# Kernel optimization log

Hardware: AMD Instinct MI355X
Metric: run time of the kernel (lower is better)

## Reference

```python
import jax, jax.numpy as jnp
import numpy as np
import math

D_MODEL = 1024
N_HEAD = 16
Q_DIM = K_DIM = V_DIM = 1024
SCALE = math.sqrt(D_MODEL // N_HEAD)  # 8.0
B, LQ, LK = 2, 2048, 2048


def setup_inputs() -> dict:
    key = jax.random.key(0)
    ks = jax.random.split(key, 10)
    s = 1.0 / math.sqrt(Q_DIM)
    return {
        "q": jax.random.normal(ks[0], (B, LQ, Q_DIM), jnp.float32),
        "k": jax.random.normal(ks[1], (B, LK, K_DIM), jnp.float32),
        "v": jax.random.normal(ks[2], (B, LK, V_DIM), jnp.float32),
        "mask": jax.random.randint(ks[3], (B, LQ, LK), 0, 2, jnp.int32),
        "Wq": jax.random.uniform(ks[4], (D_MODEL, Q_DIM), jnp.float32, -s, s),
        "bq": jnp.zeros((D_MODEL,), jnp.float32),
        "Wk": jax.random.uniform(ks[5], (D_MODEL, K_DIM), jnp.float32, -s, s),
        "bk": jnp.zeros((D_MODEL,), jnp.float32),
        "Wv": jax.random.uniform(ks[6], (D_MODEL, V_DIM), jnp.float32, -s, s),
        "bv": jnp.zeros((D_MODEL,), jnp.float32),
    }


def reference(q, k, v, Wq, bq, Wk, bk, Wv, bv, mask):
    b, lq, _ = q.shape
    lk = k.shape[1]
    dh = D_MODEL // N_HEAD
    # linear projections (torch Linear: x @ W.T + b)
    qh = (q @ Wq.T + bq).reshape(b, lq, N_HEAD, dh).transpose(0, 2, 1, 3)  # bhqd
    kh = (k @ Wk.T + bk).reshape(b, lk, N_HEAD, dh).transpose(0, 2, 1, 3)  # bhkd
    vh = (v @ Wv.T + bv).reshape(b, lk, N_HEAD, dh).transpose(0, 2, 1, 3)  # bhkd
    attn = jnp.einsum("bhqd,bhkd->bhqk", qh, kh) / SCALE
    m = mask[:, None, :, :]  # b1qk
    attn = jnp.where(m == 0, -jnp.inf, attn)
    # rows whose mask is all-zero are reset to 0 pre-softmax (-> uniform weights)
    row_empty = (m.sum(-1, keepdims=True) == 0)
    attn = jnp.where(row_empty, 0.0, attn)
    attn = jax.nn.softmax(attn, axis=-1)  # dropout is identity in eval mode
    v_out = jnp.einsum("bhqk,bhkd->bhqd", attn, vh)
    v_out = v_out.transpose(0, 2, 1, 3).reshape(b, lq, D_MODEL)
    k_out = jnp.einsum("bhqk,bhkd->bhqd", attn, kh)
    k_out = k_out.transpose(0, 2, 1, 3).reshape(b, lq, D_MODEL)
    return (k_out, v_out)
```

## Files before the change

### kernel.cpp

```cpp
#include <hip/hip_runtime.h>
#include <hip/hip_bf16.h>
#include <stdint.h>

typedef __bf16 bf16x8 __attribute__((ext_vector_type(8)));
typedef __bf16 bf16x4 __attribute__((ext_vector_type(4)));
typedef float f32x4 __attribute__((ext_vector_type(4)));

#define B_ 2
#define LQ_ 2048
#define LK_ 2048
#define NH_ 16
#define DH_ 64
#define DM_ 1024
#define NKT_ (LK_ / 64)

#define AS1 __attribute__((address_space(1)))
#define AS3 __attribute__((address_space(3)))

__device__ __forceinline__ void gload_lds16(const void* g, void* l) {
  __builtin_amdgcn_global_load_lds((const AS1 uint32_t*)g, (AS3 uint32_t*)l, 16, 0, 0);
}

__global__ __launch_bounds__(256) void prep_kernel(
    const float* __restrict__ q, const float* __restrict__ k,
    const float* __restrict__ v, const float* __restrict__ wq,
    const float* __restrict__ wk, const float* __restrict__ wv,
    const int* __restrict__ mask,
    __bf16* __restrict__ Xt0, __bf16* __restrict__ Xt1, __bf16* __restrict__ Xt2,
    __bf16* __restrict__ Wt0, __bf16* __restrict__ Wt1, __bf16* __restrict__ Wt2,
    unsigned* __restrict__ maskp) {
  const int t = threadIdx.x;
  const int bidx = blockIdx.x;
  if (bidx >= 960) {
    int pb = bidx - 960;
    int lane = t & 63;
    size_t gi = ((size_t)pb * 256 + t) * 4;
    int4 mv = *(const int4*)(mask + gi);
    unsigned nib = (mv.x != 0 ? 1u : 0u) | (mv.y != 0 ? 2u : 0u) |
                   (mv.z != 0 ? 4u : 0u) | (mv.w != 0 ? 8u : 0u);
    unsigned vv = nib << ((lane & 7) * 4);
    vv |= __shfl_xor(vv, 1, 64);
    vv |= __shfl_xor(vv, 2, 64);
    vv |= __shfl_xor(vv, 4, 64);
    if ((lane & 7) == 0) maskp[gi >> 5] = vv;
    return;
  }
  __shared__ __align__(16) __bf16 lb[16][1032];
  const float* src; __bf16* dst; int rows, m0;
  if (bidx < 256)      { src = q;  dst = Xt0; rows = 4096; m0 = bidx * 16; }
  else if (bidx < 512) { src = k;  dst = Xt1; rows = 4096; m0 = (bidx - 256) * 16; }
  else if (bidx < 768) { src = v;  dst = Xt2; rows = 4096; m0 = (bidx - 512) * 16; }
  else if (bidx < 832) { src = wq; dst = Wt0; rows = 1024; m0 = (bidx - 768) * 16; }
  else if (bidx < 896) { src = wk; dst = Wt1; rows = 1024; m0 = (bidx - 832) * 16; }
  else                 { src = wv; dst = Wt2; rows = 1024; m0 = (bidx - 896) * 16; }
#pragma unroll
  for (int i = 0; i < 16; i++) {
    float4 f = *(const float4*)(src + (size_t)(m0 + i) * DM_ + t * 4);
    bf16x4 o;
    o[0] = (__bf16)f.x; o[1] = (__bf16)f.y; o[2] = (__bf16)f.z; o[3] = (__bf16)f.w;
    *(bf16x4*)&lb[i][t * 4] = o;
  }
  __syncthreads();
  const int wave = t >> 6, lane = t & 63;
  const int m = lane >> 2, c = lane & 3;
#pragma unroll
  for (int j = 0; j < 8; j++) {
    int kt = wave * 8 + j;
    bf16x8 val = *(const bf16x8*)&lb[m][kt * 32 + (c ^ (m & 3)) * 8];
    *(bf16x8*)(dst + ((size_t)kt * rows + m0 + m) * 32 + c * 8) = val;
  }
}

__global__ __launch_bounds__(256) void proj_kernel(
    const __bf16* __restrict__ Xt0, const __bf16* __restrict__ Xt1,
    const __bf16* __restrict__ Xt2,
    const float* __restrict__ b0p, const float* __restrict__ b1p,
    const float* __restrict__ b2p,
    const __bf16* __restrict__ Wt0, const __bf16* __restrict__ Wt1,
    const __bf16* __restrict__ Wt2,
    __bf16* __restrict__ qh, __bf16* __restrict__ kh,
    __bf16* __restrict__ khT, __bf16* __restrict__ vhT) {
  __shared__ __align__(16) __bf16 smem[2][2][128 * 32];
  __bf16* cbuf = &smem[0][0][0];

  const int mode = blockIdx.z;
  const __bf16* Xt = mode == 0 ? Xt0 : (mode == 1 ? Xt1 : Xt2);
  const __bf16* Wt = mode == 0 ? Wt0 : (mode == 1 ? Wt1 : Wt2);
  const float* bias = mode == 0 ? b0p : (mode == 1 ? b1p : b2p);
  __bf16* ostd = mode == 0 ? qh : (mode == 1 ? kh : nullptr);
  __bf16* otr = mode == 0 ? nullptr : (mode == 1 ? khT : vhT);
  const float osc = mode == 0 ? 0.18033688f : 1.0f;

  const int t = threadIdx.x;
  const int wave = t >> 6, lane = t & 63;
  const int lo16 = lane & 15, quad = lane >> 4;
  const int wm = wave >> 1, wn = wave & 1;
  const int m0 = blockIdx.x * 128, n0 = blockIdx.y * 128;

  f32x4 acc[4][4] = {};

  auto stage = [&](int kt, int sel) {
#pragma unroll
    for (int ii = 2 * wave; ii < 2 * wave + 2; ii++) {
      gload_lds16(Xt + ((size_t)kt * 4096 + m0 + ii * 16) * 32 + lane * 8,
                  &smem[sel][0][ii * 512]);
      gload_lds16(Wt + ((size_t)kt * 1024 + n0 + ii * 16) * 32 + lane * 8,
                  &smem[sel][1][ii * 512]);
    }
  };

  stage(0, 0);
  for (int kt = 0; kt < 32; kt++) {
    const int sel = kt & 1;
    __syncthreads();
    if (kt + 1 < 32) stage(kt + 1, sel ^ 1);
    bf16x8 af[4], bfr[4];
#pragma unroll
    for (int g = 0; g < 4; g++) {
      int ar = wm * 64 + g * 16 + lo16;
      af[g] = *(const bf16x8*)(&smem[sel][0][ar * 32 + (quad ^ (ar & 3)) * 8]);
      int br = wn * 64 + g * 16 + lo16;
      bfr[g] = *(const bf16x8*)(&smem[sel][1][br * 32 + (quad ^ (br & 3)) * 8]);
    }
#pragma unroll
    for (int gm = 0; gm < 4; gm++)
#pragma unroll
      for (int gn = 0; gn < 4; gn++)
        acc[gm][gn] =
            __builtin_amdgcn_mfma_f32_16x16x32_bf16(af[gm], bfr[gn], acc[gm][gn], 0, 0, 0);
  }

  const int b = m0 >> 11, l0 = m0 & 2047;
  for (int nhf = 0; nhf < 2; nhf++) {
    int h = (n0 >> 6) + nhf;
    int bh = b * NH_ + h;
    if (ostd) {
      __syncthreads();
      if (wn == nhf) {
#pragma unroll
        for (int gn = 0; gn < 4; gn++) {
          float bi = bias[n0 + nhf * 64 + gn * 16 + lo16];
#pragma unroll
          for (int gm = 0; gm < 4; gm++)
#pragma unroll
            for (int r = 0; r < 4; r++)
              cbuf[(wm * 64 + gm * 16 + quad * 4 + r) * 72 + gn * 16 + lo16] =
                  (__bf16)((acc[gm][gn][r] + bi) * osc);
        }
      }
      __syncthreads();
      int m = t >> 1, coff = (t & 1) * 32;
      __bf16* dst = ostd + ((size_t)bh * LQ_ + l0 + m) * DH_ + coff;
#pragma unroll
      for (int j = 0; j < 4; j++)
        *(bf16x8*)(dst + j * 8) = *(const bf16x8*)&cbuf[m * 72 + coff + j * 8];
    }
    if (otr) {
      __syncthreads();
      if (wn == nhf) {
#pragma unroll
        for (int gn = 0; gn < 4; gn++) {
          float bi = bias[n0 + nhf * 64 + gn * 16 + lo16];
#pragma unroll
          for (int gm = 0; gm < 4; gm++) {
            bf16x4 pk;
#pragma unroll
            for (int r = 0; r < 4; r++) pk[r] = (__bf16)(acc[gm][gn][r] + bi);
            *(bf16x4*)&cbuf[(gn * 16 + lo16) * 136 + wm * 64 + gm * 16 + quad * 4] = pk;
          }
        }
      }
      __syncthreads();
      int d = t >> 2, mc = (t & 3) * 32;
      int kti = (l0 + mc) >> 6, kl = (l0 + mc) & 63;
      __bf16* dst = otr + ((size_t)(bh * NKT_ + kti) * 64 + d) * 64 + kl;
#pragma unroll
      for (int j = 0; j < 4; j++)
        *(bf16x8*)(dst + j * 8) = *(const bf16x8*)&cbuf[d * 136 + mc + j * 8];
    }
  }
}

__global__ __launch_bounds__(512) void attn_kernel(
    const __bf16* __restrict__ qh, const __bf16* __restrict__ kh,
    const __bf16* __restrict__ khT, const __bf16* __restrict__ vhT,
    const unsigned* __restrict__ maskp,
    float* __restrict__ out_k, float* __restrict__ out_v) {
  __shared__ __align__(16) __bf16 kbuf[2][64 * 64];
  __shared__ __align__(16) __bf16 ktbuf[2][64 * 64];
  __shared__ __align__(16) __bf16 vtbuf[2][64 * 64];
  __shared__ __align__(16) __bf16 p_lds[8][16][72];

  const int t = threadIdx.x;
  const int wave = t >> 6, lane = t & 63;
  const int lo16 = lane & 15, quad = lane >> 4;
  const int bh = blockIdx.x;
  const int b = bh >> 4, h = bh & 15;
  const int q0 = blockIdx.y * 128 + wave * 16;
  const int srow = lane >> 3;
  const int scg = (lane & 7) ^ srow;
  const int rsw = lo16 & 7;

  bf16x8 a_q0, a_q1;
  {
    const __bf16* qrow = qh + ((size_t)bh * LQ_ + q0 + lo16) * DH_ + quad * 8;
    a_q0 = *(const bf16x8*)(qrow);
    a_q1 = *(const bf16x8*)(qrow + 32);
  }

  bf16x8 ones;
#pragma unroll
  for (int j = 0; j < 8; j++) ones[j] = (__bf16)1.0f;

  f32x4 acc_v[4] = {};
  f32x4 acc_k[4] = {};
  f32x4 acc_l = {};

  const __bf16* khb = kh + (size_t)bh * LK_ * DH_;
  const __bf16* ktb = khT + (size_t)bh * LK_ * DH_;
  const __bf16* vtb = vhT + (size_t)bh * LK_ * DH_;

  const int row_s = wave * 8 + srow;
  auto stage = [&](int kti, int sel) {
    const int tb = kti * 4096;
    gload_lds16(khb + (size_t)(kti * 64 + row_s) * DH_ + scg * 8, &kbuf[sel][wave * 512]);
    gload_lds16(ktb + tb + row_s * 64 + scg * 8, &ktbuf[sel][wave * 512]);
    gload_lds16(vtb + tb + row_s * 64 + scg * 8, &vtbuf[sel][wave * 512]);
  };

  const unsigned* mrow = maskp + ((size_t)b * LQ_ + q0 + lo16) * (LK_ / 32);
  unsigned mw0 = mrow[0], mw1 = mrow[1];

  stage(0, 0);
  for (int kti = 0; kti < NKT_; kti++) {
    const int cur = kti & 1;
    __syncthreads();
    if (kti + 1 < NKT_) stage(kti + 1, cur ^ 1);

    unsigned nm0 = 0, nm1 = 0;
    if (kti + 1 < NKT_) {
      nm0 = mrow[(kti + 1) * 2];
      nm1 = mrow[(kti + 1) * 2 + 1];
    }

    __builtin_amdgcn_s_setprio(1);
    f32x4 s[4];
#pragma unroll
    for (int gg = 0; gg < 4; gg++) {
      int row = gg * 16 + lo16;
      bf16x8 kb0 = *(const bf16x8*)(&kbuf[cur][row * 64 + ((quad ^ rsw) * 8)]);
      bf16x8 kb1 = *(const bf16x8*)(&kbuf[cur][row * 64 + (((quad + 4) ^ rsw) * 8)]);
      f32x4 z = {};
      z = __builtin_amdgcn_mfma_f32_16x16x32_bf16(kb0, a_q0, z, 0, 0, 0);
      z = __builtin_amdgcn_mfma_f32_16x16x32_bf16(kb1, a_q1, z, 0, 0, 0);
      s[gg] = z;
    }
    __builtin_amdgcn_s_setprio(0);

#pragma unroll
    for (int gg = 0; gg < 4; gg++) {
      unsigned w = (gg >= 2) ? mw1 : mw0;
      bf16x4 pk;
#pragma unroll
      for (int r = 0; r < 4; r++) {
        int bitpos = (gg & 1) * 16 + quad * 4 + r;
        float pe = __builtin_amdgcn_exp2f(s[gg][r]);
        pk[r] = ((w >> bitpos) & 1) ? (__bf16)pe : (__bf16)0.0f;
      }
      *(bf16x4*)&p_lds[wave][lo16][gg * 16 + quad * 4] = pk;
    }
    bf16x8 a_p0 = *(const bf16x8*)&p_lds[wave][lo16][quad * 8];
    bf16x8 a_p1 = *(const bf16x8*)&p_lds[wave][lo16][32 + quad * 8];

    __builtin_amdgcn_s_setprio(1);
#pragma unroll
    for (int gg = 0; gg < 4; gg++) {
      int row = gg * 16 + lo16;
      bf16x8 bv0 = *(const bf16x8*)(&vtbuf[cur][row * 64 + ((quad ^ rsw) * 8)]);
      bf16x8 bv1 = *(const bf16x8*)(&vtbuf[cur][row * 64 + (((quad + 4) ^ rsw) * 8)]);
      bf16x8 bk0 = *(const bf16x8*)(&ktbuf[cur][row * 64 + ((quad ^ rsw) * 8)]);
      bf16x8 bk1 = *(const bf16x8*)(&ktbuf[cur][row * 64 + (((quad + 4) ^ rsw) * 8)]);
      acc_v[gg] = __builtin_amdgcn_mfma_f32_16x16x32_bf16(a_p0, bv0, acc_v[gg], 0, 0, 0);
      acc_v[gg] = __builtin_amdgcn_mfma_f32_16x16x32_bf16(a_p1, bv1, acc_v[gg], 0, 0, 0);
      acc_k[gg] = __builtin_amdgcn_mfma_f32_16x16x32_bf16(a_p0, bk0, acc_k[gg], 0, 0, 0);
      acc_k[gg] = __builtin_amdgcn_mfma_f32_16x16x32_bf16(a_p1, bk1, acc_k[gg], 0, 0, 0);
    }
    acc_l = __builtin_amdgcn_mfma_f32_16x16x32_bf16(a_p0, ones, acc_l, 0, 0, 0);
    acc_l = __builtin_amdgcn_mfma_f32_16x16x32_bf16(a_p1, ones, acc_l, 0, 0, 0);
    __builtin_amdgcn_s_setprio(0);

    mw0 = nm0;
    mw1 = nm1;
  }

  float inv_l[4];
#pragma unroll
  for (int r = 0; r < 4; r++) inv_l[r] = 1.0f / acc_l[r];
  size_t obase = ((size_t)b * LQ_ + q0 + quad * 4) * DM_ + h * DH_;
#pragma unroll
  for (int gg = 0; gg < 4; gg++) {
#pragma unroll
    for (int r = 0; r < 4; r++) {
      size_t idx = obase + (size_t)r * DM_ + gg * 16 + lo16;
      out_k[idx] = acc_k[gg][r] * inv_l[r];
      out_v[idx] = acc_v[gg][r] * inv_l[r];
    }
  }
}

extern "C" void kernel_launch(void* const* d_in, const int* in_sizes, int n_in,
                              void* d_out, int out_size, void* d_ws, size_t ws_size,
                              hipStream_t stream) {
  const float* q = (const float*)d_in[0];
  const float* k = (const float*)d_in[1];
  const float* v = (const float*)d_in[2];
  const int* mask = (const int*)d_in[3];
  const float* Wq = (const float*)d_in[4];
  const float* bq = (const float*)d_in[5];
  const float* Wk = (const float*)d_in[6];
  const float* bk = (const float*)d_in[7];
  const float* Wv = (const float*)d_in[8];
  const float* bv = (const float*)d_in[9];
  float* out = (float*)d_out;

  const size_t HTOT = (size_t)B_ * NH_ * LQ_ * DH_;
  const size_t XTOT = (size_t)B_ * LQ_ * DM_;
  const size_t MASKW = (size_t)B_ * LQ_ * (LK_ / 32);
  __bf16* qh = (__bf16*)d_ws;
  __bf16* kh = qh + HTOT;
  __bf16* khT = kh + HTOT;
  __bf16* vhT = khT + HTOT;
  unsigned* maskp = (unsigned*)(vhT + HTOT);

  const size_t SCR_ELEMS = 3 * XTOT + 3 * (size_t)DM_ * DM_;
  const size_t NEED = 4 * HTOT * sizeof(__bf16) + MASKW * sizeof(unsigned) +
                      SCR_ELEMS * sizeof(__bf16);
  __bf16* scr = (ws_size >= NEED) ? (__bf16*)(maskp + MASKW) : (__bf16*)d_out;
  __bf16* Xt0 = scr;
  __bf16* Xt1 = Xt0 + XTOT;
  __bf16* Xt2 = Xt1 + XTOT;
  __bf16* Wt0 = Xt2 + XTOT;
  __bf16* Wt1 = Wt0 + (size_t)DM_ * DM_;
  __bf16* Wt2 = Wt1 + (size_t)DM_ * DM_;

  prep_kernel<<<960 + 8192, 256, 0, stream>>>(
      q, k, v, Wq, Wk, Wv, mask, Xt0, Xt1, Xt2, Wt0, Wt1, Wt2, maskp);
  proj_kernel<<<dim3(32, 8, 3), 256, 0, stream>>>(
      Xt0, Xt1, Xt2, bq, bk, bv, Wt0, Wt1, Wt2, qh, kh, khT, vhT);
  attn_kernel<<<dim3(32, 16), 512, 0, stream>>>(qh, kh, khT, vhT, maskp,
                                                out, out + (size_t)B_ * LQ_ * DM_);
}
```

Baseline: 255.4 us.

## Load transposed K and V tiles directly from global into registers, bypassing LDS

Removes the LDS staging buffers for the transposed K and V tiles. Each wave now reads its MFMA B operands straight from global memory, with the first group issued before the softmax step and the next group prefetched during each MFMA group. This cuts shared-memory footprint and LDS traffic, but every wave re-reads the same tile from global/L2. Global-load latency is also no longer hidden by the double-buffered async copy.

```diff
diff --git a/kernel.cpp b/kernel.cpp
--- a/kernel.cpp
+++ b/kernel.cpp
@@ -187,8 +187,6 @@
     const unsigned* __restrict__ maskp,
     float* __restrict__ out_k, float* __restrict__ out_v) {
   __shared__ __align__(16) __bf16 kbuf[2][64 * 64];
-  __shared__ __align__(16) __bf16 ktbuf[2][64 * 64];
-  __shared__ __align__(16) __bf16 vtbuf[2][64 * 64];
   __shared__ __align__(16) __bf16 p_lds[8][16][72];
 
   const int t = threadIdx.x;
@@ -222,10 +220,7 @@
 
   const int row_s = wave * 8 + srow;
   auto stage = [&](int kti, int sel) {
-    const int tb = kti * 4096;
     gload_lds16(khb + (size_t)(kti * 64 + row_s) * DH_ + scg * 8, &kbuf[sel][wave * 512]);
-    gload_lds16(ktb + tb + row_s * 64 + scg * 8, &ktbuf[sel][wave * 512]);
-    gload_lds16(vtb + tb + row_s * 64 + scg * 8, &vtbuf[sel][wave * 512]);
   };
 
   const unsigned* mrow = maskp + ((size_t)b * LQ_ + q0 + lo16) * (LK_ / 32);
@@ -257,6 +252,13 @@
     }
     __builtin_amdgcn_s_setprio(0);
 
+    const __bf16* vt_t = vtb + (size_t)kti * 4096;
+    const __bf16* kt_t = ktb + (size_t)kti * 4096;
+    bf16x8 bv0 = *(const bf16x8*)(vt_t + lo16 * 64 + quad * 8);
+    bf16x8 bv1 = *(const bf16x8*)(vt_t + lo16 * 64 + 32 + quad * 8);
+    bf16x8 bk0 = *(const bf16x8*)(kt_t + lo16 * 64 + quad * 8);
+    bf16x8 bk1 = *(const bf16x8*)(kt_t + lo16 * 64 + 32 + quad * 8);
+
 #pragma unroll
     for (int gg = 0; gg < 4; gg++) {
       unsigned w = (gg >= 2) ? mw1 : mw0;
@@ -275,15 +277,18 @@
     __builtin_amdgcn_s_setprio(1);
 #pragma unroll
     for (int gg = 0; gg < 4; gg++) {
-      int row = gg * 16 + lo16;
-      bf16x8 bv0 = *(const bf16x8*)(&vtbuf[cur][row * 64 + ((quad ^ rsw) * 8)]);
-      bf16x8 bv1 = *(const bf16x8*)(&vtbuf[cur][row * 64 + (((quad + 4) ^ rsw) * 8)]);
-      bf16x8 bk0 = *(const bf16x8*)(&ktbuf[cur][row * 64 + ((quad ^ rsw) * 8)]);
-      bf16x8 bk1 = *(const bf16x8*)(&ktbuf[cur][row * 64 + (((quad + 4) ^ rsw) * 8)]);
-      acc_v[gg] = __builtin_amdgcn_mfma_f32_16x16x32_bf16(a_p0, bv0, acc_v[gg], 0, 0, 0);
-      acc_v[gg] = __builtin_amdgcn_mfma_f32_16x16x32_bf16(a_p1, bv1, acc_v[gg], 0, 0, 0);
-      acc_k[gg] = __builtin_amdgcn_mfma_f32_16x16x32_bf16(a_p0, bk0, acc_k[gg], 0, 0, 0);
-      acc_k[gg] = __builtin_amdgcn_mfma_f32_16x16x32_bf16(a_p1, bk1, acc_k[gg], 0, 0, 0);
+      bf16x8 cv0 = bv0, cv1 = bv1, ck0 = bk0, ck1 = bk1;
+      if (gg + 1 < 4) {
+        int row = (gg + 1) * 16 + lo16;
+        bv0 = *(const bf16x8*)(vt_t + row * 64 + quad * 8);
+        bv1 = *(const bf16x8*)(vt_t + row * 64 + 32 + quad * 8);
+        bk0 = *(const bf16x8*)(kt_t + row * 64 + quad * 8);
+        bk1 = *(const bf16x8*)(kt_t + row * 64 + 32 + quad * 8);
+      }
+      acc_v[gg] = __builtin_amdgcn_mfma_f32_16x16x32_bf16(a_p0, cv0, acc_v[gg], 0, 0, 0);
+      acc_v[gg] = __builtin_amdgcn_mfma_f32_16x16x32_bf16(a_p1, cv1, acc_v[gg], 0, 0, 0);
+      acc_k[gg] = __builtin_amdgcn_mfma_f32_16x16x32_bf16(a_p0, ck0, acc_k[gg], 0, 0, 0);
+      acc_k[gg] = __builtin_amdgcn_mfma_f32_16x16x32_bf16(a_p1, ck1, acc_k[gg], 0, 0, 0);
     }
     acc_l = __builtin_amdgcn_mfma_f32_16x16x32_bf16(a_p0, ones, acc_l, 0, 0, 0);
     acc_l = __builtin_amdgcn_mfma_f32_16x16x32_bf16(a_p1, ones, acc_l, 0, 0, 0);
```

Result: slower. 434.2 us (+70.0%).
